# Kernel optimization log

Measured on AMD Instinct MI355X. Metric: run time of the kernel, lower is better.

## Reference

```python
import jax, jax.numpy as jnp
import numpy as np

DIM = 768
NUM_HEADS = 12
HEAD_DIM = DIM // NUM_HEADS
SCALE = HEAD_DIM ** -0.5


def setup_inputs() -> dict:
    key = jax.random.key(0)
    k_x, k_qw, k_qb, k_pw, k_pb = jax.random.split(key, 5)
    B, N = 4, 2048
    x = jax.random.normal(k_x, (B, N, DIM), dtype=jnp.float32)
    s = 1.0 / np.sqrt(DIM)
    qkv_w = jax.random.normal(k_qw, (3 * DIM, DIM), dtype=jnp.float32) * s
    qkv_b = jax.random.normal(k_qb, (3 * DIM,), dtype=jnp.float32) * 0.02
    proj_w = jax.random.normal(k_pw, (DIM, DIM), dtype=jnp.float32) * s
    proj_b = jax.random.normal(k_pb, (DIM,), dtype=jnp.float32) * 0.02
    return {"x": x, "qkv_w": qkv_w, "qkv_b": qkv_b, "proj_w": proj_w, "proj_b": proj_b}


def reference(x, qkv_w, qkv_b, proj_w, proj_b):
    B, N, D = x.shape
    H, Hd = NUM_HEADS, HEAD_DIM
    # qkv linear: [B,N,3D] -> [3,B,H,N,Hd]
    qkv = (x @ qkv_w.T + qkv_b).reshape(B, N, 3, H, Hd).transpose(2, 0, 3, 1, 4)
    q, k, v = qkv[0], qkv[1], qkv[2]
    scores = jnp.einsum("bhnd,bhmd->bhnm", q, k) * SCALE  # [B,H,N,N]
    attn = jax.nn.softmax(scores, axis=-1)
    out = jnp.einsum("bhnm,bhmd->bhnd", attn, v)  # [B,H,N,Hd]
    out = out.transpose(0, 2, 1, 3).reshape(B, N, D)
    return out @ proj_w.T + proj_b
```

## Files before the change

### kernel.cpp

```cpp
#include <hip/hip_runtime.h>

#define SEQ 2048
#define NB 4
#define NH 12
#define DHEAD 64
#define DMODEL 768
#define D3 2304
#define MTOT 8192
#define QSCALE 0.18033688011112042f

typedef float f4v __attribute__((ext_vector_type(4)));
typedef float fl4 __attribute__((ext_vector_type(4)));
typedef short s8v __attribute__((ext_vector_type(8)));
typedef __bf16 b8v __attribute__((ext_vector_type(8)));
typedef unsigned int ui4 __attribute__((ext_vector_type(4)));
typedef unsigned int ui2 __attribute__((ext_vector_type(2)));
typedef unsigned short us4 __attribute__((ext_vector_type(4)));

#define GLDS16(g, l)                                                            \
  __builtin_amdgcn_global_load_lds(                                             \
      (const __attribute__((address_space(1))) void*)(g),                       \
      (__attribute__((address_space(3))) void*)(l), 16, 0, 0)

__device__ inline float fast_exp2(float x) {
#if __has_builtin(__builtin_amdgcn_exp2f)
  return __builtin_amdgcn_exp2f(x);
#else
  float r;
  asm("v_exp_f32 %0, %1" : "=v"(r) : "v"(x));
  return r;
#endif
}

template <typename T>
__device__ inline auto mfma_try(T a, T b, f4v c, int)
    -> decltype(__builtin_amdgcn_mfma_f32_16x16x32_bf16(a, b, c, 0, 0, 0)) {
  return __builtin_amdgcn_mfma_f32_16x16x32_bf16(a, b, c, 0, 0, 0);
}
template <typename T>
__device__ inline f4v mfma_try(T a, T b, f4v c, long) {
  return __builtin_amdgcn_mfma_f32_16x16x32_bf16(
      __builtin_bit_cast(b8v, a), __builtin_bit_cast(b8v, b), c, 0, 0, 0);
}
__device__ inline f4v mfma16(s8v a, s8v b, f4v c) { return mfma_try(a, b, c, 0); }

__device__ inline unsigned short f2bf(float f) {
  union { float f; unsigned u; } v; v.f = f;
  unsigned r = v.u + 0x7FFFu + ((v.u >> 16) & 1u);
  return (unsigned short)(r >> 16);
}

__device__ inline unsigned pack2(float a, float b) {
  unsigned ua = __builtin_bit_cast(unsigned, a) + 0x8000u;
  unsigned ub = __builtin_bit_cast(unsigned, b) + 0x8000u;
  return __builtin_amdgcn_perm(ub, ua, 0x07060302u);
}

#define NX4 1572864
#define NW14 442368
#define NW24 147456
__global__ void k_cvt(const float* __restrict__ x, const float* __restrict__ w1,
                      const float* __restrict__ w2, unsigned short* __restrict__ ox,
                      unsigned short* __restrict__ o1, unsigned short* __restrict__ o2) {
  int i = blockIdx.x * 256 + threadIdx.x;
  const float* src;
  unsigned short* dst;
  int off;
  if (i < NX4) { src = x; dst = ox; off = i; }
  else if (i < NX4 + NW14) { src = w1; dst = o1; off = i - NX4; }
  else if (i < NX4 + NW14 + NW24) { src = w2; dst = o2; off = i - NX4 - NW14; }
  else return;
  fl4 f = ((const fl4*)src)[off];
  us4 o;
  o[0] = f2bf(f[0]); o[1] = f2bf(f[1]); o[2] = f2bf(f[2]); o[3] = f2bf(f[3]);
  ((us4*)dst)[off] = o;
}

__global__ __launch_bounds__(256, 3) void k_qkv(
    const unsigned short* __restrict__ xb,
    const unsigned short* __restrict__ wb,
    const float* __restrict__ qkv_b,
    unsigned short* __restrict__ outQ,
    unsigned short* __restrict__ outK,
    unsigned short* __restrict__ outV) {
  __shared__ unsigned short As[128 * 64];
  __shared__ unsigned short Bs[128 * 64];
  const int tid = threadIdx.x;
  const int lane = tid & 63;
  const int wave = tid >> 6;
  const int wr = wave >> 1, wc = wave & 1;
  const int lr = lane & 15, lq = lane >> 4;
  const int srow = wave * 8 + (lane >> 3);
  const int scol = ((lane & 7) ^ ((lane >> 3) & 7)) * 8;
  const int swz = (lr & 7);
  const int bx = blockIdx.x;

  if (bx < 768) {
    const int rowBase = (bx >> 6) * 128;
    const int colBase = (bx & 63) * 128;
    f4v acc[4][4];
#pragma unroll
    for (int i = 0; i < 4; ++i)
#pragma unroll
      for (int j = 0; j < 4; ++j) acc[i][j] = f4v{0.f, 0.f, 0.f, 0.f};

    const unsigned short* Ag0 = wb + (long)(rowBase + srow) * DMODEL + scol;
    const unsigned short* Bg0 = xb + (long)(colBase + srow) * DMODEL + scol;
    unsigned short* Al0 = &As[srow * 64 + (lane & 7) * 8];
    unsigned short* Bl0 = &Bs[srow * 64 + (lane & 7) * 8];

    for (int kt = 0; kt < DMODEL / 64; ++kt) {
#pragma unroll
      for (int p = 0; p < 4; ++p) {
        GLDS16(Ag0 + kt * 64 + p * 32 * DMODEL, Al0 + p * 32 * 64);
        GLDS16(Bg0 + kt * 64 + p * 32 * DMODEL, Bl0 + p * 32 * 64);
      }
      __syncthreads();
#pragma unroll
      for (int ks = 0; ks < 2; ++ks) {
        s8v af[4], bf[4];
#pragma unroll
        for (int i = 0; i < 4; ++i)
          af[i] = *(const s8v*)&As[(wr * 64 + i * 16 + lr) * 64 + ((ks * 4 + lq) ^ swz) * 8];
#pragma unroll
        for (int j = 0; j < 4; ++j)
          bf[j] = *(const s8v*)&Bs[(wc * 64 + j * 16 + lr) * 64 + ((ks * 4 + lq) ^ swz) * 8];
#pragma unroll
        for (int i = 0; i < 4; ++i)
#pragma unroll
          for (int j = 0; j < 4; ++j) acc[i][j] = mfma16(af[i], bf[j], acc[i][j]);
      }
      __syncthreads();
    }

    const int fw = rowBase + wr * 64;
    fl4 bv[4];
#pragma unroll
    for (int i = 0; i < 4; ++i) bv[i] = *(const fl4*)&qkv_b[fw + i * 16 + lq * 4];
    const int isQ = fw < DMODEL;
    const int h = (fw >> 6) % NH;
    unsigned short* outQK = (unsigned short*)(isQ ? outQ : outK);
    const float scl = isQ ? QSCALE : 1.0f;
#pragma unroll
    for (int j = 0; j < 4; ++j) {
      const int ng = colBase + wc * 64 + j * 16 + lr;
      const int b = ng >> 11, nn = ng & 2047;
#pragma unroll
      for (int i = 0; i < 4; ++i) {
        float v0 = (acc[i][j][0] + bv[i][0]) * scl, v1 = (acc[i][j][1] + bv[i][1]) * scl;
        float v2 = (acc[i][j][2] + bv[i][2]) * scl, v3 = (acc[i][j][3] + bv[i][3]) * scl;
        *(ui2*)(outQK + (long)(((b * NH + h) * SEQ) + nn) * DHEAD + (i * 16 + lq * 4)) =
            ui2{pack2(v0, v1), pack2(v2, v3)};
      }
    }
  } else {
    const int vb = bx - 768;
    const int rowBase = (vb / 12) * 128;
    const int colBase = (vb % 12) * 64;
    f4v acc[4][2];
#pragma unroll
    for (int i = 0; i < 4; ++i)
#pragma unroll
      for (int j = 0; j < 2; ++j) acc[i][j] = f4v{0.f, 0.f, 0.f, 0.f};

    const unsigned short* Ag0 = xb + (long)(rowBase + srow) * DMODEL + scol;
    const unsigned short* Bg0 =
        wb + (long)(2 * DMODEL + colBase + srow) * DMODEL + scol;
    unsigned short* Al0 = &As[srow * 64 + (lane & 7) * 8];
    unsigned short* Bl0 = &Bs[srow * 64 + (lane & 7) * 8];

    for (int kt = 0; kt < DMODEL / 64; ++kt) {
#pragma unroll
      for (int p = 0; p < 4; ++p)
        GLDS16(Ag0 + kt * 64 + p * 32 * DMODEL, Al0 + p * 32 * 64);
#pragma unroll
      for (int p = 0; p < 2; ++p)
        GLDS16(Bg0 + kt * 64 + p * 32 * DMODEL, Bl0 + p * 32 * 64);
      __syncthreads();
#pragma unroll
      for (int ks = 0; ks < 2; ++ks) {
        s8v af[4], bf[2];
#pragma unroll
        for (int i = 0; i < 4; ++i)
          af[i] = *(const s8v*)&As[(wr * 64 + i * 16 + lr) * 64 + ((ks * 4 + lq) ^ swz) * 8];
#pragma unroll
        for (int j = 0; j < 2; ++j)
          bf[j] = *(const s8v*)&Bs[(wc * 32 + j * 16 + lr) * 64 + ((ks * 4 + lq) ^ swz) * 8];
#pragma unroll
        for (int i = 0; i < 4; ++i)
#pragma unroll
          for (int j = 0; j < 2; ++j) acc[i][j] = mfma16(af[i], bf[j], acc[i][j]);
      }
      __syncthreads();
    }

#pragma unroll
    for (int j = 0; j < 2; ++j) {
      const int col = colBase + wc * 32 + j * 16 + lr;
      const float bvs = qkv_b[2 * DMODEL + col];
      const int h = col >> 6, hd = col & 63;
#pragma unroll
      for (int i = 0; i < 4; ++i) {
        const int row = rowBase + wr * 64 + i * 16 + lq * 4;
        const int b = row >> 11, n = row & 2047;
        const int bq = (n >> 2) & 7;
        const int np = (n & ~31) + ((bq & 3) << 3) + ((bq >> 2) << 2);
        float v0 = acc[i][j][0] + bvs, v1 = acc[i][j][1] + bvs;
        float v2 = acc[i][j][2] + bvs, v3 = acc[i][j][3] + bvs;
        *(ui2*)&outV[(long)(((b * NH + h) * DHEAD) + hd) * SEQ + np] =
            ui2{pack2(v0, v1), pack2(v2, v3)};
      }
    }
  }
}

__global__ __launch_bounds__(256, 3) void k_proj(
    const unsigned short* __restrict__ Wp,
    const unsigned short* __restrict__ Xt,
    const float* __restrict__ bias,
    float* __restrict__ outF) {
  __shared__ unsigned short As[128 * 64];
  __shared__ unsigned short Bs[64 * 64];
  const int tid = threadIdx.x;
  const int lane = tid & 63;
  const int wave = tid >> 6;
  const int wr = wave >> 1, wc = wave & 1;
  const int lr = lane & 15, lq = lane >> 4;
  const int srow = wave * 8 + (lane >> 3);
  const int scol = ((lane & 7) ^ ((lane >> 3) & 7)) * 8;
  const int swz = (lr & 7);
  const int rowBase = blockIdx.y * 128;
  const int colBase = blockIdx.x * 64;

  f4v acc[4][2];
#pragma unroll
  for (int i = 0; i < 4; ++i)
#pragma unroll
    for (int j = 0; j < 2; ++j) acc[i][j] = f4v{0.f, 0.f, 0.f, 0.f};

  const unsigned short* Ag0 = Wp + (long)(rowBase + srow) * DMODEL + scol;
  const unsigned short* Bg0 = Xt + (long)(colBase + srow) * DMODEL + scol;
  unsigned short* Al0 = &As[srow * 64 + (lane & 7) * 8];
  unsigned short* Bl0 = &Bs[srow * 64 + (lane & 7) * 8];

  for (int kt = 0; kt < DMODEL / 64; ++kt) {
#pragma unroll
    for (int p = 0; p < 4; ++p)
      GLDS16(Ag0 + kt * 64 + p * 32 * DMODEL, Al0 + p * 32 * 64);
#pragma unroll
    for (int p = 0; p < 2; ++p)
      GLDS16(Bg0 + kt * 64 + p * 32 * DMODEL, Bl0 + p * 32 * 64);
    __syncthreads();
#pragma unroll
    for (int ks = 0; ks < 2; ++ks) {
      s8v af[4], bf[2];
#pragma unroll
      for (int i = 0; i < 4; ++i)
        af[i] = *(const s8v*)&As[(wr * 64 + i * 16 + lr) * 64 + ((ks * 4 + lq) ^ swz) * 8];
#pragma unroll
      for (int j = 0; j < 2; ++j)
        bf[j] = *(const s8v*)&Bs[(wc * 32 + j * 16 + lr) * 64 + ((ks * 4 + lq) ^ swz) * 8];
#pragma unroll
      for (int i = 0; i < 4; ++i)
#pragma unroll
        for (int j = 0; j < 2; ++j) acc[i][j] = mfma16(af[i], bf[j], acc[i][j]);
    }
    __syncthreads();
  }

  const int fw = rowBase + wr * 64;
  fl4 bv[4];
#pragma unroll
  for (int i = 0; i < 4; ++i) bv[i] = *(const fl4*)&bias[fw + i * 16 + lq * 4];
#pragma unroll
  for (int j = 0; j < 2; ++j) {
    const int ng = colBase + wc * 32 + j * 16 + lr;
#pragma unroll
    for (int i = 0; i < 4; ++i) {
      float v0 = acc[i][j][0] + bv[i][0], v1 = acc[i][j][1] + bv[i][1];
      float v2 = acc[i][j][2] + bv[i][2], v3 = acc[i][j][3] + bv[i][3];
      *(fl4*)&outF[(long)ng * DMODEL + fw + i * 16 + lq * 4] = fl4{v0, v1, v2, v3};
    }
  }
}

__global__ __launch_bounds__(256, 3) void k_attn(
    const unsigned short* __restrict__ Q,
    const unsigned short* __restrict__ Kg,
    const unsigned short* __restrict__ Vt,
    unsigned short* __restrict__ Ob) {
  __shared__ unsigned short Ks[128 * 64];
  __shared__ unsigned short Vs[64 * 128];
  const int tid = threadIdx.x;
  const int lane = tid & 63;
  const int wave = tid >> 6;
  const int lr = lane & 15;
  const int lq = lane >> 4;
  const int bh = blockIdx.y;
  const int b = bh / NH, h = bh % NH;
  const int q0 = blockIdx.x * 128;
  const unsigned short* Qb = Q + (long)bh * SEQ * DHEAD;
  const unsigned short* Kb = Kg + (long)bh * SEQ * DHEAD;
  const unsigned short* Vb = Vt + (long)bh * DHEAD * SEQ;

  s8v qf[2][2];
#pragma unroll
  for (int i = 0; i < 2; ++i)
#pragma unroll
    for (int ss = 0; ss < 2; ++ss)
      qf[i][ss] = *(const s8v*)(Qb + (q0 + wave * 32 + i * 16 + lr) * DHEAD + ss * 32 + lq * 8);

  f4v o[2][4];
  f4v la[2] = {f4v{0.f, 0.f, 0.f, 0.f}, f4v{0.f, 0.f, 0.f, 0.f}};
  const f4v zc = f4v{0.f, 0.f, 0.f, 0.f};
  const s8v ones = {0x3F80, 0x3F80, 0x3F80, 0x3F80, 0x3F80, 0x3F80, 0x3F80, 0x3F80};
#pragma unroll
  for (int i = 0; i < 2; ++i)
#pragma unroll
    for (int jo = 0; jo < 4; ++jo) o[i][jo] = f4v{0.f, 0.f, 0.f, 0.f};

  const int srow = wave * 8 + (lane >> 3);
  const int scol = ((lane & 7) ^ ((lane >> 3) & 7)) * 8;
  const unsigned short* Kg0 = Kb + (long)srow * DHEAD + scol;
  unsigned short* Kl0 = &Ks[srow * 64 + (lane & 7) * 8];
  const int swz = (lr & 7);
  const int vdrow = wave * 4 + (lane >> 4);
  const int vchunk = (lane & 15) ^ vdrow;
  const unsigned short* Vg0 = Vb + (long)vdrow * SEQ + vchunk * 8;
  unsigned short* Vl0 = &Vs[vdrow * 128 + (lane & 15) * 8];

  for (int kt = 0; kt < SEQ / 128; ++kt) {
#pragma unroll
    for (int p = 0; p < 4; ++p)
      GLDS16(Kg0 + (long)(kt * 128 + p * 32) * DHEAD, Kl0 + p * 32 * 64);
#pragma unroll
    for (int p = 0; p < 4; ++p)
      GLDS16(Vg0 + (long)(p * 16) * SEQ + kt * 128, Vl0 + p * 16 * 128);
    __syncthreads();

    f4v s[2][8];
#pragma unroll
    for (int t = 0; t < 8; ++t) {
      s8v kf0 = *(const s8v*)&Ks[(t * 16 + lr) * 64 + ((0 * 4 + lq) ^ swz) * 8];
      s8v kf1 = *(const s8v*)&Ks[(t * 16 + lr) * 64 + ((1 * 4 + lq) ^ swz) * 8];
      s[0][t] = mfma16(kf0, qf[0][0], zc);
      s[1][t] = mfma16(kf0, qf[1][0], zc);
      s[0][t] = mfma16(kf1, qf[0][1], s[0][t]);
      s[1][t] = mfma16(kf1, qf[1][1], s[1][t]);
    }

    unsigned pk[2][8][2];
#pragma unroll
    for (int i = 0; i < 2; ++i)
#pragma unroll
      for (int t = 0; t < 8; ++t) {
        float p0 = fast_exp2(s[i][t][0]);
        float p1 = fast_exp2(s[i][t][1]);
        float p2 = fast_exp2(s[i][t][2]);
        float p3 = fast_exp2(s[i][t][3]);
        pk[i][t][0] = pack2(p0, p1);
        pk[i][t][1] = pack2(p2, p3);
      }

#pragma unroll
    for (int ss = 0; ss < 4; ++ss) {
      s8v vf[4];
#pragma unroll
      for (int jo = 0; jo < 4; ++jo)
        vf[jo] = *(const s8v*)&Vs[(jo * 16 + lr) * 128 + ((ss * 4 + lq) ^ lr) * 8];
#pragma unroll
      for (int i = 0; i < 2; ++i) {
        s8v pf = __builtin_bit_cast(
            s8v, ui4{pk[i][2 * ss][0], pk[i][2 * ss][1], pk[i][2 * ss + 1][0], pk[i][2 * ss + 1][1]});
        la[i] = mfma16(ones, pf, la[i]);
#pragma unroll
        for (int jo = 0; jo < 4; ++jo) o[i][jo] = mfma16(vf[jo], pf, o[i][jo]);
      }
    }
    __syncthreads();
  }

  float linv[2];
  linv[0] = 1.0f / la[0][0];
  linv[1] = 1.0f / la[1][0];

#pragma unroll
  for (int i = 0; i < 2; ++i) {
    const long nrow = (long)(b * SEQ + q0 + wave * 32 + i * 16 + lr) * DMODEL;
#pragma unroll
    for (int jo = 0; jo < 4; ++jo) {
      float v0 = o[i][jo][0] * linv[i];
      float v1 = o[i][jo][1] * linv[i];
      float v2 = o[i][jo][2] * linv[i];
      float v3 = o[i][jo][3] * linv[i];
      *(ui2*)(Ob + nrow + h * DHEAD + jo * 16 + lq * 4) = ui2{pack2(v0, v1), pack2(v2, v3)};
    }
  }
}

extern "C" void kernel_launch(void* const* d_in, const int* in_sizes, int n_in,
                              void* d_out, int out_size, void* d_ws, size_t ws_size,
                              hipStream_t stream) {
  (void)in_sizes; (void)n_in; (void)out_size; (void)ws_size;
  const float* x = (const float*)d_in[0];
  const float* qkv_w = (const float*)d_in[1];
  const float* qkv_b = (const float*)d_in[2];
  const float* proj_w = (const float*)d_in[3];
  const float* proj_b = (const float*)d_in[4];
  float* out = (float*)d_out;

  unsigned short* ws = (unsigned short*)d_ws;
  unsigned short* xb = ws;
  unsigned short* wqkvb = xb + 6291456;
  unsigned short* wprjb = wqkvb + 1769472;
  unsigned short* qb = wprjb + 589824;
  unsigned short* kb = qb + 6291456;
  unsigned short* vtb = kb + 6291456;
  unsigned short* aob = vtb + 6291456;

  k_cvt<<<(NX4 + NW14 + NW24 + 255) / 256, 256, 0, stream>>>(
      x, qkv_w, proj_w, xb, wqkvb, wprjb);

  k_qkv<<<1536, 256, 0, stream>>>(xb, wqkvb, qkv_b, qb, kb, vtb);
  k_attn<<<dim3(SEQ / 128, NB * NH), 256, 0, stream>>>(qb, kb, vtb, aob);
  k_proj<<<dim3(MTOT / 64, DMODEL / 128), 256, 0, stream>>>(wprjb, aob, proj_b, out);
}
```

Baseline: 202.6 us.

## Fuse all stages into one cooperative persistent kernel with grid syncs

Replaces the four separate launches (convert, QKV GEMM, attention, projection) with a single cooperative kernel. It sizes the grid from the occupancy query and loops each block over the work items of each stage, separated by grid-wide syncs. The aim is to remove launch gaps and inter-kernel drain/fill between stages. The cost is grid-sync overhead, possible load imbalance when the job counts do not divide evenly over the resident blocks, and an extra hipOccupancy query on every call. A fallback to the separate kernels remains if the cooperative launch fails.

New measurement: 404.8 us. 2x slower.

```diff
diff --git a/kernel.cpp b/kernel.cpp
--- a/kernel.cpp
+++ b/kernel.cpp
@@ -1,4 +1,7 @@
 #include <hip/hip_runtime.h>
+#include <hip/hip_cooperative_groups.h>
+
+namespace cg = cooperative_groups;
 
 #define SEQ 2048
 #define NB 4
@@ -59,32 +62,35 @@
 #define NX4 1572864
 #define NW14 442368
 #define NW24 147456
-__global__ void k_cvt(const float* __restrict__ x, const float* __restrict__ w1,
-                      const float* __restrict__ w2, unsigned short* __restrict__ ox,
-                      unsigned short* __restrict__ o1, unsigned short* __restrict__ o2) {
-  int i = blockIdx.x * 256 + threadIdx.x;
+#define NCVT (NX4 + NW14 + NW24)
+
+__device__ inline void cvt_elem(int i, const float* __restrict__ x,
+                                const float* __restrict__ w1,
+                                const float* __restrict__ w2,
+                                unsigned short* __restrict__ ox,
+                                unsigned short* __restrict__ o1,
+                                unsigned short* __restrict__ o2) {
   const float* src;
   unsigned short* dst;
   int off;
   if (i < NX4) { src = x; dst = ox; off = i; }
   else if (i < NX4 + NW14) { src = w1; dst = o1; off = i - NX4; }
-  else if (i < NX4 + NW14 + NW24) { src = w2; dst = o2; off = i - NX4 - NW14; }
-  else return;
+  else { src = w2; dst = o2; off = i - NX4 - NW14; }
   fl4 f = ((const fl4*)src)[off];
   us4 o;
   o[0] = f2bf(f[0]); o[1] = f2bf(f[1]); o[2] = f2bf(f[2]); o[3] = f2bf(f[3]);
   ((us4*)dst)[off] = o;
 }
 
-__global__ __launch_bounds__(256, 3) void k_qkv(
-    const unsigned short* __restrict__ xb,
-    const unsigned short* __restrict__ wb,
-    const float* __restrict__ qkv_b,
-    unsigned short* __restrict__ outQ,
-    unsigned short* __restrict__ outK,
-    unsigned short* __restrict__ outV) {
-  __shared__ unsigned short As[128 * 64];
-  __shared__ unsigned short Bs[128 * 64];
+__device__ inline void qkv_job(unsigned short* sm, int bxj,
+                               const unsigned short* __restrict__ xb,
+                               const unsigned short* __restrict__ wb,
+                               const float* __restrict__ qkv_b,
+                               unsigned short* __restrict__ outQ,
+                               unsigned short* __restrict__ outK,
+                               unsigned short* __restrict__ outV) {
+  unsigned short* As = sm;
+  unsigned short* Bs = sm + 8192;
   const int tid = threadIdx.x;
   const int lane = tid & 63;
   const int wave = tid >> 6;
@@ -93,11 +99,10 @@
   const int srow = wave * 8 + (lane >> 3);
   const int scol = ((lane & 7) ^ ((lane >> 3) & 7)) * 8;
   const int swz = (lr & 7);
-  const int bx = blockIdx.x;
-
-  if (bx < 768) {
-    const int rowBase = (bx >> 6) * 128;
-    const int colBase = (bx & 63) * 128;
+
+  if (bxj < 768) {
+    const int rowBase = (bxj >> 6) * 128;
+    const int colBase = (bxj & 63) * 128;
     f4v acc[4][4];
 #pragma unroll
     for (int i = 0; i < 4; ++i)
@@ -139,7 +144,7 @@
     for (int i = 0; i < 4; ++i) bv[i] = *(const fl4*)&qkv_b[fw + i * 16 + lq * 4];
     const int isQ = fw < DMODEL;
     const int h = (fw >> 6) % NH;
-    unsigned short* outQK = (unsigned short*)(isQ ? outQ : outK);
+    unsigned short* outQK = isQ ? outQ : outK;
     const float scl = isQ ? QSCALE : 1.0f;
 #pragma unroll
     for (int j = 0; j < 4; ++j) {
@@ -154,7 +159,7 @@
       }
     }
   } else {
-    const int vb = bx - 768;
+    const int vb = bxj - 768;
     const int rowBase = (vb / 12) * 128;
     const int colBase = (vb % 12) * 64;
     f4v acc[4][2];
@@ -164,8 +169,7 @@
       for (int j = 0; j < 2; ++j) acc[i][j] = f4v{0.f, 0.f, 0.f, 0.f};
 
     const unsigned short* Ag0 = xb + (long)(rowBase + srow) * DMODEL + scol;
-    const unsigned short* Bg0 =
-        wb + (long)(2 * DMODEL + colBase + srow) * DMODEL + scol;
+    const unsigned short* Bg0 = wb + (long)(2 * DMODEL + colBase + srow) * DMODEL + scol;
     unsigned short* Al0 = &As[srow * 64 + (lane & 7) * 8];
     unsigned short* Bl0 = &Bs[srow * 64 + (lane & 7) * 8];
 
@@ -214,91 +218,21 @@
   }
 }
 
-__global__ __launch_bounds__(256, 3) void k_proj(
-    const unsigned short* __restrict__ Wp,
-    const unsigned short* __restrict__ Xt,
-    const float* __restrict__ bias,
-    float* __restrict__ outF) {
-  __shared__ unsigned short As[128 * 64];
-  __shared__ unsigned short Bs[64 * 64];
-  const int tid = threadIdx.x;
-  const int lane = tid & 63;
-  const int wave = tid >> 6;
-  const int wr = wave >> 1, wc = wave & 1;
-  const int lr = lane & 15, lq = lane >> 4;
-  const int srow = wave * 8 + (lane >> 3);
-  const int scol = ((lane & 7) ^ ((lane >> 3) & 7)) * 8;
-  const int swz = (lr & 7);
-  const int rowBase = blockIdx.y * 128;
-  const int colBase = blockIdx.x * 64;
-
-  f4v acc[4][2];
-#pragma unroll
-  for (int i = 0; i < 4; ++i)
-#pragma unroll
-    for (int j = 0; j < 2; ++j) acc[i][j] = f4v{0.f, 0.f, 0.f, 0.f};
-
-  const unsigned short* Ag0 = Wp + (long)(rowBase + srow) * DMODEL + scol;
-  const unsigned short* Bg0 = Xt + (long)(colBase + srow) * DMODEL + scol;
-  unsigned short* Al0 = &As[srow * 64 + (lane & 7) * 8];
-  unsigned short* Bl0 = &Bs[srow * 64 + (lane & 7) * 8];
-
-  for (int kt = 0; kt < DMODEL / 64; ++kt) {
-#pragma unroll
-    for (int p = 0; p < 4; ++p)
-      GLDS16(Ag0 + kt * 64 + p * 32 * DMODEL, Al0 + p * 32 * 64);
-#pragma unroll
-    for (int p = 0; p < 2; ++p)
-      GLDS16(Bg0 + kt * 64 + p * 32 * DMODEL, Bl0 + p * 32 * 64);
-    __syncthreads();
-#pragma unroll
-    for (int ks = 0; ks < 2; ++ks) {
-      s8v af[4], bf[2];
-#pragma unroll
-      for (int i = 0; i < 4; ++i)
-        af[i] = *(const s8v*)&As[(wr * 64 + i * 16 + lr) * 64 + ((ks * 4 + lq) ^ swz) * 8];
-#pragma unroll
-      for (int j = 0; j < 2; ++j)
-        bf[j] = *(const s8v*)&Bs[(wc * 32 + j * 16 + lr) * 64 + ((ks * 4 + lq) ^ swz) * 8];
-#pragma unroll
-      for (int i = 0; i < 4; ++i)
-#pragma unroll
-        for (int j = 0; j < 2; ++j) acc[i][j] = mfma16(af[i], bf[j], acc[i][j]);
-    }
-    __syncthreads();
-  }
-
-  const int fw = rowBase + wr * 64;
-  fl4 bv[4];
-#pragma unroll
-  for (int i = 0; i < 4; ++i) bv[i] = *(const fl4*)&bias[fw + i * 16 + lq * 4];
-#pragma unroll
-  for (int j = 0; j < 2; ++j) {
-    const int ng = colBase + wc * 32 + j * 16 + lr;
-#pragma unroll
-    for (int i = 0; i < 4; ++i) {
-      float v0 = acc[i][j][0] + bv[i][0], v1 = acc[i][j][1] + bv[i][1];
-      float v2 = acc[i][j][2] + bv[i][2], v3 = acc[i][j][3] + bv[i][3];
-      *(fl4*)&outF[(long)ng * DMODEL + fw + i * 16 + lq * 4] = fl4{v0, v1, v2, v3};
-    }
-  }
-}
-
-__global__ __launch_bounds__(256, 3) void k_attn(
-    const unsigned short* __restrict__ Q,
-    const unsigned short* __restrict__ Kg,
-    const unsigned short* __restrict__ Vt,
-    unsigned short* __restrict__ Ob) {
-  __shared__ unsigned short Ks[128 * 64];
-  __shared__ unsigned short Vs[64 * 128];
+__device__ inline void attn_block(unsigned short* sm, int bx,
+                                  const unsigned short* __restrict__ Q,
+                                  const unsigned short* __restrict__ Kg,
+                                  const unsigned short* __restrict__ Vt,
+                                  unsigned short* __restrict__ Ob) {
+  unsigned short* Ks = sm;
+  unsigned short* Vs = sm + 8192;
   const int tid = threadIdx.x;
   const int lane = tid & 63;
   const int wave = tid >> 6;
   const int lr = lane & 15;
   const int lq = lane >> 4;
-  const int bh = blockIdx.y;
+  const int bh = bx >> 4;
   const int b = bh / NH, h = bh % NH;
-  const int q0 = blockIdx.x * 128;
+  const int q0 = (bx & 15) * 128;
   const unsigned short* Qb = Q + (long)bh * SEQ * DHEAD;
   const unsigned short* Kb = Kg + (long)bh * SEQ * DHEAD;
   const unsigned short* Vb = Vt + (long)bh * DHEAD * SEQ;
@@ -396,6 +330,130 @@
       *(ui2*)(Ob + nrow + h * DHEAD + jo * 16 + lq * 4) = ui2{pack2(v0, v1), pack2(v2, v3)};
     }
   }
+}
+
+__device__ inline void proj_block(unsigned short* sm, int bx,
+                                  const unsigned short* __restrict__ Wp,
+                                  const unsigned short* __restrict__ Xt,
+                                  const float* __restrict__ bias,
+                                  float* __restrict__ outF) {
+  unsigned short* As = sm;
+  unsigned short* Bs = sm + 8192;
+  const int tid = threadIdx.x;
+  const int lane = tid & 63;
+  const int wave = tid >> 6;
+  const int wr = wave >> 1, wc = wave & 1;
+  const int lr = lane & 15, lq = lane >> 4;
+  const int srow = wave * 8 + (lane >> 3);
+  const int scol = ((lane & 7) ^ ((lane >> 3) & 7)) * 8;
+  const int swz = (lr & 7);
+  const int rowBase = (bx >> 7) * 128;
+  const int colBase = (bx & 127) * 64;
+
+  f4v acc[4][2];
+#pragma unroll
+  for (int i = 0; i < 4; ++i)
+#pragma unroll
+    for (int j = 0; j < 2; ++j) acc[i][j] = f4v{0.f, 0.f, 0.f, 0.f};
+
+  const unsigned short* Ag0 = Wp + (long)(rowBase + srow) * DMODEL + scol;
+  const unsigned short* Bg0 = Xt + (long)(colBase + srow) * DMODEL + scol;
+  unsigned short* Al0 = &As[srow * 64 + (lane & 7) * 8];
+  unsigned short* Bl0 = &Bs[srow * 64 + (lane & 7) * 8];
+
+  for (int kt = 0; kt < DMODEL / 64; ++kt) {
+#pragma unroll
+    for (int p = 0; p < 4; ++p)
+      GLDS16(Ag0 + kt * 64 + p * 32 * DMODEL, Al0 + p * 32 * 64);
+#pragma unroll
+    for (int p = 0; p < 2; ++p)
+      GLDS16(Bg0 + kt * 64 + p * 32 * DMODEL, Bl0 + p * 32 * 64);
+    __syncthreads();
+#pragma unroll
+    for (int ks = 0; ks < 2; ++ks) {
+      s8v af[4], bf[2];
+#pragma unroll
+      for (int i = 0; i < 4; ++i)
+        af[i] = *(const s8v*)&As[(wr * 64 + i * 16 + lr) * 64 + ((ks * 4 + lq) ^ swz) * 8];
+#pragma unroll
+      for (int j = 0; j < 2; ++j)
+        bf[j] = *(const s8v*)&Bs[(wc * 32 + j * 16 + lr) * 64 + ((ks * 4 + lq) ^ swz) * 8];
+#pragma unroll
+      for (int i = 0; i < 4; ++i)
+#pragma unroll
+        for (int j = 0; j < 2; ++j) acc[i][j] = mfma16(af[i], bf[j], acc[i][j]);
+    }
+    __syncthreads();
+  }
+
+  const int fw = rowBase + wr * 64;
+  fl4 bv[4];
+#pragma unroll
+  for (int i = 0; i < 4; ++i) bv[i] = *(const fl4*)&bias[fw + i * 16 + lq * 4];
+#pragma unroll
+  for (int j = 0; j < 2; ++j) {
+    const int ng = colBase + wc * 32 + j * 16 + lr;
+#pragma unroll
+    for (int i = 0; i < 4; ++i) {
+      float v0 = acc[i][j][0] + bv[i][0], v1 = acc[i][j][1] + bv[i][1];
+      float v2 = acc[i][j][2] + bv[i][2], v3 = acc[i][j][3] + bv[i][3];
+      *(fl4*)&outF[(long)ng * DMODEL + fw + i * 16 + lq * 4] = fl4{v0, v1, v2, v3};
+    }
+  }
+}
+
+__global__ __launch_bounds__(256, 3) void k_fused(
+    const float* x, const float* w1, const float* w2,
+    const float* qkv_b, const float* proj_b,
+    unsigned short* xb, unsigned short* wqkvb, unsigned short* wprjb,
+    unsigned short* qb, unsigned short* kb, unsigned short* vtb,
+    unsigned short* aob, float* out) {
+  __shared__ unsigned short sm[16384];
+  cg::grid_group grid = cg::this_grid();
+  const int nb = gridDim.x;
+  const int bx = blockIdx.x;
+  const int tid = threadIdx.x;
+
+  for (int i = bx * 256 + tid; i < NCVT; i += nb * 256)
+    cvt_elem(i, x, w1, w2, xb, wqkvb, wprjb);
+  grid.sync();
+
+  for (int j = bx; j < 1536; j += nb)
+    qkv_job(sm, j, xb, wqkvb, qkv_b, qb, kb, vtb);
+  grid.sync();
+
+  for (int j = bx; j < 768; j += nb)
+    attn_block(sm, j, qb, kb, vtb, aob);
+  grid.sync();
+
+  for (int j = bx; j < 768; j += nb)
+    proj_block(sm, j, wprjb, aob, proj_b, out);
+}
+
+__global__ __launch_bounds__(256) void k_cvt_fb(
+    const float* __restrict__ x, const float* __restrict__ w1,
+    const float* __restrict__ w2, unsigned short* __restrict__ ox,
+    unsigned short* __restrict__ o1, unsigned short* __restrict__ o2) {
+  int i = blockIdx.x * 256 + threadIdx.x;
+  if (i < NCVT) cvt_elem(i, x, w1, w2, ox, o1, o2);
+}
+__global__ __launch_bounds__(256, 3) void k_qkv_fb(
+    const unsigned short* xb, const unsigned short* wb, const float* qkv_b,
+    unsigned short* outQ, unsigned short* outK, unsigned short* outV) {
+  __shared__ unsigned short sm[16384];
+  qkv_job(sm, blockIdx.x, xb, wb, qkv_b, outQ, outK, outV);
+}
+__global__ __launch_bounds__(256, 3) void k_attn_fb(
+    const unsigned short* Q, const unsigned short* Kg, const unsigned short* Vt,
+    unsigned short* Ob) {
+  __shared__ unsigned short sm[16384];
+  attn_block(sm, blockIdx.x, Q, Kg, Vt, Ob);
+}
+__global__ __launch_bounds__(256, 3) void k_proj_fb(
+    const unsigned short* Wp, const unsigned short* Xt, const float* bias,
+    float* outF) {
+  __shared__ unsigned short sm[16384];
+  proj_block(sm, blockIdx.x, Wp, Xt, bias, outF);
 }
 
 extern "C" void kernel_launch(void* const* d_in, const int* in_sizes, int n_in,
@@ -418,10 +476,27 @@
   unsigned short* vtb = kb + 6291456;
   unsigned short* aob = vtb + 6291456;
 
-  k_cvt<<<(NX4 + NW14 + NW24 + 255) / 256, 256, 0, stream>>>(
-      x, qkv_w, proj_w, xb, wqkvb, wprjb);
-
-  k_qkv<<<1536, 256, 0, stream>>>(xb, wqkvb, qkv_b, qb, kb, vtb);
-  k_attn<<<dim3(SEQ / 128, NB * NH), 256, 0, stream>>>(qb, kb, vtb, aob);
-  k_proj<<<dim3(MTOT / 64, DMODEL / 128), 256, 0, stream>>>(wprjb, aob, proj_b, out);
-}
+  int occ = 0;
+  hipError_t qe = hipOccupancyMaxActiveBlocksPerMultiprocessor(
+      &occ, (const void*)k_fused, 256, 0);
+  int nblk = 0;
+  if (qe == hipSuccess && occ > 0) {
+    nblk = occ * 256;
+    if (nblk > 768) nblk = 768;
+  }
+
+  hipError_t le = hipErrorUnknown;
+  if (nblk >= 256) {
+    void* args[] = {&x, &qkv_w, &proj_w, &qkv_b, &proj_b,
+                    &xb, &wqkvb, &wprjb, &qb, &kb, &vtb, &aob, &out};
+    le = hipLaunchCooperativeKernel((void*)k_fused, dim3(nblk), dim3(256), args,
+                                    0, stream);
+  }
+  if (le != hipSuccess) {
+    (void)hipGetLastError();
+    k_cvt_fb<<<(NCVT + 255) / 256, 256, 0, stream>>>(x, qkv_w, proj_w, xb, wqkvb, wprjb);
+    k_qkv_fb<<<1536, 256, 0, stream>>>(xb, wqkvb, qkv_b, qb, kb, vtb);
+    k_attn_fb<<<768, 256, 0, stream>>>(qb, kb, vtb, aob);
+    k_proj_fb<<<768, 256, 0, stream>>>(wprjb, aob, proj_b, out);
+  }
+}
```
